# Optimization experiments

Hardware: AMD Instinct MI355X
Metric: run time of the kernel (lower is better)

The kernel has to match this reference:

```python
import jax, jax.numpy as jnp
from jax import lax
import numpy as np

B, T = 256, 64
VOCAB, EMB, UNITS = 10000, 256, 512


def _lstm(x, mask, Wi, Wh, b, reverse, return_sequences):
    # x: [B,T,D], mask: [B,T] bool. Keras LSTM: act=tanh, rec_act=sigmoid,
    # gate order i,f,c,o. Masked steps carry state (output = previous output).
    Bsz = x.shape[0]
    U = Wh.shape[0]
    xw = jnp.einsum('btd,dg->btg', x, Wi) + b  # precompute input projections

    def step(carry, inp):
        h, c = carry
        xw_t, m_t = inp  # [B,4U], [B,1]
        z = xw_t + h @ Wh
        i, f, g, o = jnp.split(z, 4, axis=-1)
        c_new = jax.nn.sigmoid(f) * c + jax.nn.sigmoid(i) * jnp.tanh(g)
        h_new = jax.nn.sigmoid(o) * jnp.tanh(c_new)
        h = jnp.where(m_t, h_new, h)
        c = jnp.where(m_t, c_new, c)
        return (h, c), h

    init = (jnp.zeros((Bsz, U), x.dtype), jnp.zeros((Bsz, U), x.dtype))
    xs = (xw.transpose(1, 0, 2), mask.T[:, :, None])
    (h, _), ys = lax.scan(step, init, xs, reverse=reverse)
    return ys.transpose(1, 0, 2) if return_sequences else h


def _bilstm(x, mask, fwd, bwd, return_sequences):
    yf = _lstm(x, mask, *fwd, reverse=False, return_sequences=return_sequences)
    yb = _lstm(x, mask, *bwd, reverse=True, return_sequences=return_sequences)
    return jnp.concatenate([yf, yb], axis=-1)


def setup_inputs() -> dict:
    key = jax.random.key(0)
    ks = jax.random.split(key, 24)
    g = lambda k, shp, s=0.05: jax.random.normal(k, shp, dtype=jnp.float32) * s
    d = {
        'encoder_output': jax.random.normal(ks[0], (B, 10, 10, 2048), dtype=jnp.float32),
        'sequences': jax.random.randint(ks[1], (B, T), 0, VOCAB),
        'emb': g(ks[2], (VOCAB, EMB)),
        'l1f_Wi': g(ks[3], (EMB, 4 * UNITS)), 'l1f_Wh': g(ks[4], (UNITS, 4 * UNITS)), 'l1f_b': jnp.zeros((4 * UNITS,), jnp.float32),
        'l1b_Wi': g(ks[5], (EMB, 4 * UNITS)), 'l1b_Wh': g(ks[6], (UNITS, 4 * UNITS)), 'l1b_b': jnp.zeros((4 * UNITS,), jnp.float32),
        'l2f_Wi': g(ks[7], (2 * UNITS, 4 * UNITS)), 'l2f_Wh': g(ks[8], (UNITS, 4 * UNITS)), 'l2f_b': jnp.zeros((4 * UNITS,), jnp.float32),
        'l2b_Wi': g(ks[9], (2 * UNITS, 4 * UNITS)), 'l2b_Wh': g(ks[10], (UNITS, 4 * UNITS)), 'l2b_b': jnp.zeros((4 * UNITS,), jnp.float32),
        'W1': g(ks[11], (2048 + 2 * UNITS, 1024)), 'b1': jnp.zeros((1024,), jnp.float32),
        'W2': g(ks[12], (1024, 512)), 'b2': jnp.zeros((512,), jnp.float32),
        'W3': g(ks[13], (512, 1)), 'b3': jnp.zeros((1,), jnp.float32),
    }
    return d


def reference(encoder_output, sequences, emb,
              l1f_Wi, l1f_Wh, l1f_b, l1b_Wi, l1b_Wh, l1b_b,
              l2f_Wi, l2f_Wh, l2f_b, l2b_Wi, l2b_Wh, l2b_b,
              W1, b1, W2, b2, W3, b3):
    # training=False: all dropout layers are identity.
    pooled = jnp.mean(encoder_output, axis=(1, 2))  # [B, 2048]
    mask = sequences != 0                            # mask_zero=True
    tok = emb[sequences]                             # [B,T,EMB]
    lstm1_out = _bilstm(tok, mask, (l1f_Wi, l1f_Wh, l1f_b), (l1b_Wi, l1b_Wh, l1b_b), True)
    lstm2_out = _bilstm(lstm1_out, mask, (l2f_Wi, l2f_Wh, l2f_b), (l2b_Wi, l2b_Wh, l2b_b), False)
    feats = jnp.concatenate([pooled, lstm2_out], axis=1)  # [B, 3072]
    x = jax.nn.relu(feats @ W1 + b1)
    x = jax.nn.relu(x @ W2 + b2)
    return jax.nn.sigmoid(x @ W3 + b3)  # [B,1]
```

## Files before the change

kernel.cpp:

```cpp
#include <hip/hip_runtime.h>
#include <hip/hip_bf16.h>
#include <math.h>

#define BB 256
#define TT 64
#define UU 512
#define XWD 33554432
#define WSTR 520

typedef __hip_bfloat16 bf16;
typedef __attribute__((ext_vector_type(8))) short sh8;
typedef __attribute__((ext_vector_type(4))) short sh4;
typedef __attribute__((ext_vector_type(4))) float floatx4;
typedef __attribute__((ext_vector_type(4))) unsigned int ui4;

__device__ __forceinline__ float bf2f(short s) {
    union { unsigned int u; float f; } v;
    v.u = ((unsigned int)(unsigned short)s) << 16;
    return v.f;
}
__device__ __forceinline__ short f2bf_bits(float f) {
    union { float f; unsigned u; } v; v.f = f;
    unsigned rr = v.u + 0x7fff + ((v.u >> 16) & 1);
    return (short)(rr >> 16);
}
__device__ __forceinline__ float fsig(float x)  { return 1.0f / (1.0f + __expf(-x)); }
__device__ __forceinline__ float ftanh(float x) { return 2.0f / (1.0f + __expf(-2.0f * x)) - 1.0f; }

union U16 { ui4 u; sh8 s; };

__device__ __forceinline__ void coh_load_h8(const bf16* p, sh8 hv[8]) {
    U16 a0, a1, a2, a3, a4, a5, a6, a7;
    asm volatile(
        "global_load_dwordx4 %[o0], %[ad], off sc0 sc1\n\t"
        "global_load_dwordx4 %[o1], %[ad], off offset:64 sc0 sc1\n\t"
        "global_load_dwordx4 %[o2], %[ad], off offset:128 sc0 sc1\n\t"
        "global_load_dwordx4 %[o3], %[ad], off offset:192 sc0 sc1\n\t"
        "global_load_dwordx4 %[o4], %[ad], off offset:256 sc0 sc1\n\t"
        "global_load_dwordx4 %[o5], %[ad], off offset:320 sc0 sc1\n\t"
        "global_load_dwordx4 %[o6], %[ad], off offset:384 sc0 sc1\n\t"
        "global_load_dwordx4 %[o7], %[ad], off offset:448 sc0 sc1\n\t"
        "s_waitcnt vmcnt(0)"
        : [o0]"=&v"(a0.u), [o1]"=&v"(a1.u), [o2]"=&v"(a2.u), [o3]"=&v"(a3.u),
          [o4]"=&v"(a4.u), [o5]"=&v"(a5.u), [o6]"=&v"(a6.u), [o7]"=&v"(a7.u)
        : [ad]"v"(p)
        : "memory");
    hv[0] = a0.s; hv[1] = a1.s; hv[2] = a2.s; hv[3] = a3.s;
    hv[4] = a4.s; hv[5] = a5.s; hv[6] = a6.s; hv[7] = a7.s;
}
__device__ __forceinline__ void coh_store_h(bf16* p, short v) {
    asm volatile("global_store_short %[ad], %[dv], off sc0 sc1"
                 :: [ad]"v"(p), [dv]"v"((unsigned)(unsigned short)v) : "memory");
}
__device__ __forceinline__ void flag_store(unsigned* p, unsigned v) {
    asm volatile("global_store_dword %[ad], %[dv], off sc0 sc1"
                 :: [ad]"v"(p), [dv]"v"(v) : "memory");
}
__device__ __forceinline__ unsigned flag_load(const unsigned* p) {
    unsigned v;
    asm volatile("global_load_dword %[dv], %[ad], off sc0 sc1\n\t"
                 "s_waitcnt vmcnt(0)"
                 : [dv]"=&v"(v) : [ad]"v"(p) : "memory");
    return v;
}

#define GLDS(gp, lp) __builtin_amdgcn_global_load_lds( \
    (const __attribute__((address_space(1))) unsigned int*)(const void*)(gp), \
    (__attribute__((address_space(3))) unsigned int*)(void*)(lp), 16, 0, 0)

__global__ void transpose_conv_kernel(const float* __restrict__ in, bf16* __restrict__ out,
                                      int K, int N, int out_stride) {
    __shared__ float tile[32][33];
    int k0 = blockIdx.y * 32;
    int n0 = blockIdx.x * 32;
    int tid = threadIdx.x;
    int nn = tid & 31, kk = tid >> 5;
    #pragma unroll
    for (int j = 0; j < 4; ++j)
        tile[kk + j * 8][nn] = in[(size_t)(k0 + kk + j * 8) * N + n0 + nn];
    __syncthreads();
    int kk2 = tid & 31, nn2 = tid >> 5;
    #pragma unroll
    for (int j = 0; j < 4; ++j)
        out[(size_t)(n0 + nn2 + j * 8) * out_stride + k0 + kk2] =
            __float2bfloat16(tile[kk2][nn2 + j * 8]);
}

__global__ void pool_kernel(const float* __restrict__ enc, float* __restrict__ pooled) {
    int b = blockIdx.y;
    int e = blockIdx.x * 256 + threadIdx.x;
    const float* p = enc + (size_t)b * 100 * 2048 + e;
    float s = 0.f;
    #pragma unroll 4
    for (int i = 0; i < 100; ++i) s += p[(size_t)i * 2048];
    pooled[(size_t)b * 2048 + e] = s * 0.01f;
}

__global__ void embed_kernel(const int* __restrict__ seq, const float* __restrict__ emb,
                             bf16* __restrict__ tok) {
    int i = blockIdx.x;
    int e = threadIdx.x;
    int b = i >> 6, t = i & 63;
    tok[((size_t)t * BB + b) * 256 + e] = __float2bfloat16(emb[(size_t)seq[i] * 256 + e]);
}

__global__ __launch_bounds__(256)
void gemm_tile(const bf16* __restrict__ A, const bf16* __restrict__ Wt,
               const float* __restrict__ bias, bf16* __restrict__ out,
               int M, int N, int K, int relu, int mode) {
    __shared__ __align__(16) bf16 As[128 * 32];
    __shared__ __align__(16) bf16 Bs[128 * 32];
    const int tid = threadIdx.x;
    const int w = tid >> 6, lane = tid & 63;
    const int lm = lane & 15, q = lane >> 4;
    const int m0 = blockIdx.y * 128;
    const int n0 = blockIdx.x * 128;
    const int wm = (w & 1) * 64, wn = (w >> 1) * 64;

    const int srow = tid >> 2;
    const int sk8  = (tid & 3) * 8;
    const bf16* ga0 = A  + (size_t)(m0 + srow) * K + sk8;
    const bf16* ga1 = A  + (size_t)(m0 + 64 + srow) * K + sk8;
    const bf16* gb0 = Wt + (size_t)(n0 + srow) * K + sk8;
    const bf16* gb1 = Wt + (size_t)(n0 + 64 + srow) * K + sk8;
    bf16* la0 = As + tid * 8;
    bf16* la1 = As + 2048 + tid * 8;
    bf16* lb0 = Bs + tid * 8;
    bf16* lb1 = Bs + 2048 + tid * 8;

    floatx4 acc[4][4];
    #pragma unroll
    for (int i = 0; i < 4; ++i)
        #pragma unroll
        for (int j = 0; j < 4; ++j) acc[i][j] = (floatx4){0.f, 0.f, 0.f, 0.f};

    const bf16* ra[4];
    const bf16* rb[4];
    #pragma unroll
    for (int i = 0; i < 4; ++i) ra[i] = As + (wm + i * 16 + lm) * 32 + q * 8;
    #pragma unroll
    for (int j = 0; j < 4; ++j) rb[j] = Bs + (wn + j * 16 + lm) * 32 + q * 8;

    for (int k0 = 0; k0 < K; k0 += 32) {
        GLDS(ga0 + k0, la0);
        GLDS(ga1 + k0, la1);
        GLDS(gb0 + k0, lb0);
        GLDS(gb1 + k0, lb1);
        __syncthreads();
        sh8 af[4], bfr[4];
        #pragma unroll
        for (int i = 0; i < 4; ++i) af[i] = *(const sh8*)ra[i];
        #pragma unroll
        for (int j = 0; j < 4; ++j) bfr[j] = *(const sh8*)rb[j];
        #pragma unroll
        for (int i = 0; i < 4; ++i)
            #pragma unroll
            for (int j = 0; j < 4; ++j)
                acc[i][j] = __builtin_amdgcn_mfma_f32_16x16x32_bf16(af[i], bfr[j], acc[i][j], 0, 0, 0);
        __syncthreads();
    }

    if (mode == 0) {
        #pragma unroll
        for (int i = 0; i < 4; ++i)
            #pragma unroll
            for (int j = 0; j < 4; ++j) {
                int n = n0 + wn + j * 16 + lm;
                float bv = bias[n];
                #pragma unroll
                for (int r = 0; r < 4; ++r) {
                    int m = m0 + wm + i * 16 + q * 4 + r;
                    float v = acc[i][j][r] + bv;
                    if (relu) v = fmaxf(v, 0.f);
                    out[(size_t)m * N + n] = __float2bfloat16(v);
                }
            }
    } else {
        #pragma unroll
        for (int i = 0; i < 4; ++i) {
            int mb = m0 + wm + i * 16 + q * 4;
            int t = mb >> 8;
            int bq = (mb >> 2) & 63;
            #pragma unroll
            for (int j = 0; j < 4; ++j) {
                int n = n0 + wn + j * 16 + lm;
                float bv = bias[n];
                size_t base = ((((size_t)(t * 64 + bq) * 32 + ((n >> 4) & 31)) * 16
                               + (n & 15)) * 16) + (n >> 9) * 4;
                sh4 sv;
                #pragma unroll
                for (int r = 0; r < 4; ++r)
                    sv[r] = f2bf_bits(acc[i][j][r] + bv);
                *(sh4*)(out + base) = sv;
            }
        }
    }
}

__device__ __forceinline__ void bar_arrive(unsigned* myflag, unsigned val) {
    __syncthreads();
    if (threadIdx.x == 0) flag_store(myflag, val);
}
__device__ __forceinline__ void bar_wait(unsigned* flagbase, unsigned target) {
    if (threadIdx.x < 64) {
        unsigned* my = flagbase + (threadIdx.x & 31);
        for (;;) {
            unsigned v = flag_load(my);
            if (__all(v >= target)) break;
            __builtin_amdgcn_s_sleep(1);
        }
    }
    __syncthreads();
}

__global__ __launch_bounds__(512, 2)
void lstm_seq(const bf16* __restrict__ xw, const bf16* __restrict__ Wht,
              const int* __restrict__ seq, bf16* __restrict__ h0b,
              bf16* __restrict__ h1b, bf16* __restrict__ seqout,
              unsigned* __restrict__ gflags, int tbase) {
    const int dir = blockIdx.z;
    const int u0 = blockIdx.x * 16;
    const int tid = threadIdx.x;
    const int w = tid >> 6, lane = tid & 63;
    const int lm = lane & 15, q = lane >> 4;
    const int kh = w >> 2;
    const int wb = w & 3;
    const int b0blk = blockIdx.y * 64;
    const int b0w = b0blk + wb * 16;
    unsigned* flagbase = gflags + (blockIdx.z * 4 + blockIdx.y) * 32;
    unsigned* myflag   = flagbase + blockIdx.x;

    __shared__ float part[4 * 64 * 17];
    __shared__ __align__(16) bf16 lW[64 * WSTR];
    __shared__ int sq[TT * 64];

    const size_t hdb = (size_t)dir * BB * UU;
    const int koff = kh * 256;
    const bf16* Wd = Wht + (size_t)dir * 2048 * UU;

    for (int i = tid; i < TT * 64; i += 512) {
        int tt = i >> 6, bb = i & 63;
        sq[i] = seq[(b0blk + bb) * TT + tt];
    }
    {
        int row = tid >> 3;
        int ck  = (tid & 7) * 64;
        int g = row >> 4, lmr = row & 15;
        const bf16* gsrc = Wd + (size_t)(g * UU + u0 + lmr) * UU + ck;
        bf16* ldst = lW + row * WSTR + ck;
        #pragma unroll
        for (int j = 0; j < 8; ++j)
            *(sh8*)(ldst + j * 8) = *(const sh8*)(gsrc + j * 8);
    }
    __syncthreads();

    const bf16* lwp0 = lW + (0 * 16 + lm) * WSTR + q * 8 + koff;
    const bf16* lwp1 = lW + (1 * 16 + lm) * WSTR + q * 8 + koff;
    const bf16* lwp2 = lW + (2 * 16 + lm) * WSTR + q * 8 + koff;
    const bf16* lwp3 = lW + (3 * 16 + lm) * WSTR + q * 8 + koff;

    float creg[4] = {0.f, 0.f, 0.f, 0.f};
    float hreg[4] = {0.f, 0.f, 0.f, 0.f};

    sh8 x0p = (sh8)0, x1p = (sh8)0;
    if (kh == 0) {
        const int t0s = dir ? (TT - 1) : 0;
        const bf16* xwp = xw + (size_t)dir * XWD
            + (((size_t)(t0s * 64 + (b0w >> 2) + q) * 32 + (u0 >> 4)) * 16 + lm) * 16;
        x0p = *(const sh8*)xwp;
        x1p = *(const sh8*)(xwp + 8);
    }

    for (int s = 0; s < TT; ++s) {
        const int t = dir ? (TT - 1 - s) : s;
        const bf16* hin = (s & 1) ? h1b : h0b;
        bf16*      hout = (s & 1) ? h0b : h1b;

        if (s) bar_wait(flagbase, (unsigned)(tbase + s));

        const bf16* hA = hin + hdb + (size_t)(b0w + lm) * UU + q * 8 + koff;
        sh8 hv[8];
        coh_load_h8(hA, hv);

        floatx4 acc0, acc1, acc2, acc3;
        if (kh == 0) {
            acc0 = (floatx4){bf2f(x0p[0]), bf2f(x0p[1]), bf2f(x0p[2]), bf2f(x0p[3])};
            acc1 = (floatx4){bf2f(x0p[4]), bf2f(x0p[5]), bf2f(x0p[6]), bf2f(x0p[7])};
            acc2 = (floatx4){bf2f(x1p[0]), bf2f(x1p[1]), bf2f(x1p[2]), bf2f(x1p[3])};
            acc3 = (floatx4){bf2f(x1p[4]), bf2f(x1p[5]), bf2f(x1p[6]), bf2f(x1p[7])};
        } else {
            acc0 = acc1 = acc2 = acc3 = (floatx4){0.f, 0.f, 0.f, 0.f};
        }

        #pragma unroll
        for (int kc = 0; kc < 8; ++kc) {
            sh8 a0 = *(const sh8*)(lwp0 + kc * 32);
            sh8 a1 = *(const sh8*)(lwp1 + kc * 32);
            sh8 a2 = *(const sh8*)(lwp2 + kc * 32);
            sh8 a3 = *(const sh8*)(lwp3 + kc * 32);
            acc0 = __builtin_amdgcn_mfma_f32_16x16x32_bf16(hv[kc], a0, acc0, 0, 0, 0);
            acc1 = __builtin_amdgcn_mfma_f32_16x16x32_bf16(hv[kc], a1, acc1, 0, 0, 0);
            acc2 = __builtin_amdgcn_mfma_f32_16x16x32_bf16(hv[kc], a2, acc2, 0, 0, 0);
            acc3 = __builtin_amdgcn_mfma_f32_16x16x32_bf16(hv[kc], a3, acc3, 0, 0, 0);
        }

        if (kh == 1) {
            float* pp = part + (wb * 64 + lane) * 17;
            #pragma unroll
            for (int r = 0; r < 4; ++r) {
                pp[r] = acc0[r]; pp[4 + r] = acc1[r];
                pp[8 + r] = acc2[r]; pp[12 + r] = acc3[r];
            }
        }
        __syncthreads();
        if (kh == 0) {
            const float* pp = part + (wb * 64 + lane) * 17;
            #pragma unroll
            for (int r = 0; r < 4; ++r) {
                acc0[r] += pp[r]; acc1[r] += pp[4 + r];
                acc2[r] += pp[8 + r]; acc3[r] += pp[12 + r];
            }
            const int uu = u0 + lm;
            #pragma unroll
            for (int r = 0; r < 4; ++r) {
                int b = b0w + q * 4 + r;
                bool m = (sq[t * 64 + wb * 16 + q * 4 + r] != 0);
                float cp = creg[r];
                float cn = fsig(acc1[r]) * cp + fsig(acc0[r]) * ftanh(acc2[r]);
                float hn = fsig(acc3[r]) * ftanh(cn);
                float hv2 = m ? hn : hreg[r];
                creg[r] = m ? cn : cp;
                hreg[r] = hv2;
                size_t off = hdb + (size_t)b * UU + uu;
                short hb = f2bf_bits(hv2);
                coh_store_h(&hout[off], hb);
                if (seqout)
                    __builtin_nontemporal_store(hb,
                        (short*)&seqout[((size_t)t * BB + b) * 1024 + dir * UU + uu]);
            }
        }
        bar_arrive(myflag, (unsigned)(tbase + s + 1));

        if (kh == 0 && s + 1 < TT) {
            const int tn = dir ? (TT - 2 - s) : (s + 1);
            const bf16* xwp = xw + (size_t)dir * XWD
                + (((size_t)(tn * 64 + (b0w >> 2) + q) * 32 + (u0 >> 4)) * 16 + lm) * 16;
            x0p = *(const sh8*)xwp;
            x1p = *(const sh8*)(xwp + 8);
        }
    }
}

__global__ void concat_kernel(const float* __restrict__ pooled, const bf16* __restrict__ h2,
                              bf16* __restrict__ feats) {
    int b = blockIdx.x;
    for (int j = threadIdx.x; j < 3072; j += 256) {
        bf16 v;
        if (j < 2048) v = __float2bfloat16(pooled[(size_t)b * 2048 + j]);
        else {
            int u = j - 2048;
            int dir = u >> 9;
            int uu = u & 511;
            v = h2[((size_t)dir * BB + b) * UU + uu];
        }
        feats[(size_t)b * 3072 + j] = v;
    }
}

__global__ void final_kernel(const bf16* __restrict__ x2, const float* __restrict__ W3,
                             const float* __restrict__ b3, float* __restrict__ out) {
    int b = blockIdx.x;
    int tid = threadIdx.x;
    float v = __bfloat162float(x2[(size_t)b * 512 + tid]) * W3[tid]
            + __bfloat162float(x2[(size_t)b * 512 + 256 + tid]) * W3[256 + tid];
    for (int off = 32; off > 0; off >>= 1) v += __shfl_down(v, off, 64);
    __shared__ float wsum[4];
    if ((tid & 63) == 0) wsum[tid >> 6] = v;
    __syncthreads();
    if (tid == 0) {
        float sum = wsum[0] + wsum[1] + wsum[2] + wsum[3] + b3[0];
        out[b] = 1.0f / (1.0f + expf(-sum));
    }
}

extern "C" void kernel_launch(void* const* d_in, const int* in_sizes, int n_in,
                              void* d_out, int out_size, void* d_ws, size_t ws_size,
                              hipStream_t stream) {
    const float* enc    = (const float*)d_in[0];
    const int*   seq    = (const int*)  d_in[1];
    const float* emb    = (const float*)d_in[2];
    const float* l1f_Wi = (const float*)d_in[3];
    const float* l1f_Wh = (const float*)d_in[4];
    const float* l1f_b  = (const float*)d_in[5];
    const float* l1b_Wi = (const float*)d_in[6];
    const float* l1b_Wh = (const float*)d_in[7];
    const float* l1b_b  = (const float*)d_in[8];
    const float* l2f_Wi = (const float*)d_in[9];
    const float* l2f_Wh = (const float*)d_in[10];
    const float* l2f_b  = (const float*)d_in[11];
    const float* l2b_Wi = (const float*)d_in[12];
    const float* l2b_Wh = (const float*)d_in[13];
    const float* l2b_b  = (const float*)d_in[14];
    const float* W1     = (const float*)d_in[15];
    const float* b1     = (const float*)d_in[16];
    const float* W2     = (const float*)d_in[17];
    const float* b2     = (const float*)d_in[18];
    const float* W3     = (const float*)d_in[19];
    const float* b3     = (const float*)d_in[20];

    char* p = (char*)d_ws;
    bf16* tok      = (bf16*)p;  p += (size_t)TT * BB * 256 * 2;
    bf16* lstm1out = (bf16*)p;  p += (size_t)TT * BB * 1024 * 2;
    bf16* xw       = (bf16*)p;  p += (size_t)2 * XWD * 2;
    bf16* Wh1t     = (bf16*)p;  p += (size_t)2 * 2048 * 512 * 2;
    bf16* Wh2t     = (bf16*)p;  p += (size_t)2 * 2048 * 512 * 2;
    bf16* Wi1t     = (bf16*)p;  p += (size_t)2 * 2048 * 256 * 2;
    bf16* Wi2t     = (bf16*)p;  p += (size_t)2 * 2048 * 1024 * 2;
    bf16* W1t      = (bf16*)p;  p += (size_t)1024 * 3072 * 2;
    bf16* W2t      = (bf16*)p;  p += (size_t)512 * 1024 * 2;
    float* pooled  = (float*)p; p += (size_t)BB * 2048 * 4;
    bf16* feats    = (bf16*)p;  p += (size_t)BB * 3072 * 2;
    bf16* x1       = (bf16*)p;  p += (size_t)BB * 1024 * 2;
    bf16* x2       = (bf16*)p;  p += (size_t)BB * 512 * 2;
    bf16* hb0      = (bf16*)p;  p += (size_t)2 * BB * UU * 2;
    bf16* hb1      = (bf16*)p;  p += (size_t)2 * BB * UU * 2;
    unsigned* gflags = (unsigned*)p; p += 8 * 128;

    hipMemsetAsync(gflags, 0, 8 * 128, stream);

    transpose_conv_kernel<<<dim3(64, 16), 256, 0, stream>>>(l1f_Wh, Wh1t,                    512, 2048, 512);
    transpose_conv_kernel<<<dim3(64, 16), 256, 0, stream>>>(l1b_Wh, Wh1t + (size_t)2048*512, 512, 2048, 512);
    transpose_conv_kernel<<<dim3(64, 16), 256, 0, stream>>>(l2f_Wh, Wh2t,                    512, 2048, 512);
    transpose_conv_kernel<<<dim3(64, 16), 256, 0, stream>>>(l2b_Wh, Wh2t + (size_t)2048*512, 512, 2048, 512);
    transpose_conv_kernel<<<dim3(64, 8),  256, 0, stream>>>(l1f_Wi, Wi1t,                    256, 2048, 256);
    transpose_conv_kernel<<<dim3(64, 8),  256, 0, stream>>>(l1b_Wi, Wi1t + (size_t)2048*256, 256, 2048, 256);
    transpose_conv_kernel<<<dim3(64, 32), 256, 0, stream>>>(l2f_Wi, Wi2t,                     1024, 2048, 1024);
    transpose_conv_kernel<<<dim3(64, 32), 256, 0, stream>>>(l2b_Wi, Wi2t + (size_t)2048*1024, 1024, 2048, 1024);
    transpose_conv_kernel<<<dim3(32, 96), 256, 0, stream>>>(W1, W1t, 3072, 1024, 3072);
    transpose_conv_kernel<<<dim3(16, 32), 256, 0, stream>>>(W2, W2t, 1024, 512, 1024);

    pool_kernel<<<dim3(8, BB), 256, 0, stream>>>(enc, pooled);
    embed_kernel<<<dim3(BB * TT), 256, 0, stream>>>(seq, emb, tok);

    hipMemsetAsync(hb0, 0, (size_t)2 * BB * UU * 2, stream);
    gemm_tile<<<dim3(16, 128), 256, 0, stream>>>(tok, Wi1t,                    l1f_b, xw,       16384, 2048, 256, 0, 2);
    gemm_tile<<<dim3(16, 128), 256, 0, stream>>>(tok, Wi1t + (size_t)2048*256, l1b_b, xw + XWD, 16384, 2048, 256, 0, 2);
    lstm_seq<<<dim3(32, 4, 2), 512, 0, stream>>>(xw, Wh1t, seq, hb0, hb1, lstm1out, gflags, 0);

    hipMemsetAsync(hb0, 0, (size_t)2 * BB * UU * 2, stream);
    gemm_tile<<<dim3(16, 128), 256, 0, stream>>>(lstm1out, Wi2t,                     l2f_b, xw,       16384, 2048, 1024, 0, 2);
    gemm_tile<<<dim3(16, 128), 256, 0, stream>>>(lstm1out, Wi2t + (size_t)2048*1024, l2b_b, xw + XWD, 16384, 2048, 1024, 0, 2);
    lstm_seq<<<dim3(32, 4, 2), 512, 0, stream>>>(xw, Wh2t, seq, hb0, hb1, nullptr, gflags, TT);

    concat_kernel<<<dim3(BB), 256, 0, stream>>>(pooled, hb0, feats);
    gemm_tile<<<dim3(8, 2), 256, 0, stream>>>(feats, W1t, b1, x1, BB, 1024, 3072, 1, 0);
    gemm_tile<<<dim3(4, 2), 256, 0, stream>>>(x1, W2t, b2, x2, BB, 512, 1024, 1, 0);
    final_kernel<<<dim3(BB), 256, 0, stream>>>(x2, W3, b3, (float*)d_out);
}
```

Before: 1.505 ms.

## Per-wave flag polling, deeper xw prefetch, and deferred sequence-output stores

Each wave now polls the global step flags itself instead of wave 0 polling and then a block-wide __syncthreads, which removes one block barrier per timestep. The input-projection prefetch is doubled to two timesteps ahead so the global load latency is better hidden. The nontemporal stores of the sequence output are moved after the flag arrive, which shortens the critical path before other blocks are released. In exchange, all waves hammer the flag memory (more polling traffic) and the kernel holds more registers for the second prefetch buffer.

```diff
diff --git a/kernel.cpp b/kernel.cpp
--- a/kernel.cpp
+++ b/kernel.cpp
@@ -201,16 +201,13 @@
     __syncthreads();
     if (threadIdx.x == 0) flag_store(myflag, val);
 }
-__device__ __forceinline__ void bar_wait(unsigned* flagbase, unsigned target) {
-    if (threadIdx.x < 64) {
-        unsigned* my = flagbase + (threadIdx.x & 31);
-        for (;;) {
-            unsigned v = flag_load(my);
-            if (__all(v >= target)) break;
-            __builtin_amdgcn_s_sleep(1);
-        }
-    }
-    __syncthreads();
+__device__ __forceinline__ void bar_wait_wave(unsigned* flagbase, unsigned target) {
+    unsigned* my = flagbase + (threadIdx.x & 31);
+    for (;;) {
+        unsigned v = flag_load(my);
+        if (__all(v >= target)) break;
+        __builtin_amdgcn_s_sleep(1);
+    }
 }
 
 __global__ __launch_bounds__(512, 2)
@@ -262,13 +259,17 @@
     float creg[4] = {0.f, 0.f, 0.f, 0.f};
     float hreg[4] = {0.f, 0.f, 0.f, 0.f};
 
-    sh8 x0p = (sh8)0, x1p = (sh8)0;
+    sh8 xA0 = (sh8)0, xA1 = (sh8)0, xB0 = (sh8)0, xB1 = (sh8)0;
+    const size_t xwbase = (size_t)dir * XWD;
     if (kh == 0) {
-        const int t0s = dir ? (TT - 1) : 0;
-        const bf16* xwp = xw + (size_t)dir * XWD
-            + (((size_t)(t0s * 64 + (b0w >> 2) + q) * 32 + (u0 >> 4)) * 16 + lm) * 16;
-        x0p = *(const sh8*)xwp;
-        x1p = *(const sh8*)(xwp + 8);
+        const int ta = dir ? (TT - 1) : 0;
+        const int tb = dir ? (TT - 2) : 1;
+        const bf16* pa = xw + xwbase
+            + (((size_t)(ta * 64 + (b0w >> 2) + q) * 32 + (u0 >> 4)) * 16 + lm) * 16;
+        const bf16* pb = xw + xwbase
+            + (((size_t)(tb * 64 + (b0w >> 2) + q) * 32 + (u0 >> 4)) * 16 + lm) * 16;
+        xA0 = *(const sh8*)pa;  xA1 = *(const sh8*)(pa + 8);
+        xB0 = *(const sh8*)pb;  xB1 = *(const sh8*)(pb + 8);
     }
 
     for (int s = 0; s < TT; ++s) {
@@ -276,7 +277,7 @@
         const bf16* hin = (s & 1) ? h1b : h0b;
         bf16*      hout = (s & 1) ? h0b : h1b;
 
-        if (s) bar_wait(flagbase, (unsigned)(tbase + s));
+        if (s) bar_wait_wave(flagbase, (unsigned)(tbase + s));
 
         const bf16* hA = hin + hdb + (size_t)(b0w + lm) * UU + q * 8 + koff;
         sh8 hv[8];
@@ -284,10 +285,10 @@
 
         floatx4 acc0, acc1, acc2, acc3;
         if (kh == 0) {
-            acc0 = (floatx4){bf2f(x0p[0]), bf2f(x0p[1]), bf2f(x0p[2]), bf2f(x0p[3])};
-            acc1 = (floatx4){bf2f(x0p[4]), bf2f(x0p[5]), bf2f(x0p[6]), bf2f(x0p[7])};
-            acc2 = (floatx4){bf2f(x1p[0]), bf2f(x1p[1]), bf2f(x1p[2]), bf2f(x1p[3])};
-            acc3 = (floatx4){bf2f(x1p[4]), bf2f(x1p[5]), bf2f(x1p[6]), bf2f(x1p[7])};
+            acc0 = (floatx4){bf2f(xA0[0]), bf2f(xA0[1]), bf2f(xA0[2]), bf2f(xA0[3])};
+            acc1 = (floatx4){bf2f(xA0[4]), bf2f(xA0[5]), bf2f(xA0[6]), bf2f(xA0[7])};
+            acc2 = (floatx4){bf2f(xA1[0]), bf2f(xA1[1]), bf2f(xA1[2]), bf2f(xA1[3])};
+            acc3 = (floatx4){bf2f(xA1[4]), bf2f(xA1[5]), bf2f(xA1[6]), bf2f(xA1[7])};
         } else {
             acc0 = acc1 = acc2 = acc3 = (floatx4){0.f, 0.f, 0.f, 0.f};
         }
@@ -313,6 +314,7 @@
             }
         }
         __syncthreads();
+        short hbits[4] = {0, 0, 0, 0};
         if (kh == 0) {
             const float* pp = part + (wb * 64 + lane) * 17;
             #pragma unroll
@@ -332,21 +334,30 @@
                 creg[r] = m ? cn : cp;
                 hreg[r] = hv2;
                 size_t off = hdb + (size_t)b * UU + uu;
-                short hb = f2bf_bits(hv2);
-                coh_store_h(&hout[off], hb);
-                if (seqout)
-                    __builtin_nontemporal_store(hb,
+                hbits[r] = f2bf_bits(hv2);
+                coh_store_h(&hout[off], hbits[r]);
+            }
+        }
+        bar_arrive(myflag, (unsigned)(tbase + s + 1));
+
+        if (kh == 0) {
+            if (seqout) {
+                const int uu = u0 + lm;
+                #pragma unroll
+                for (int r = 0; r < 4; ++r) {
+                    int b = b0w + q * 4 + r;
+                    __builtin_nontemporal_store(hbits[r],
                         (short*)&seqout[((size_t)t * BB + b) * 1024 + dir * UU + uu]);
-            }
-        }
-        bar_arrive(myflag, (unsigned)(tbase + s + 1));
-
-        if (kh == 0 && s + 1 < TT) {
-            const int tn = dir ? (TT - 2 - s) : (s + 1);
-            const bf16* xwp = xw + (size_t)dir * XWD
-                + (((size_t)(tn * 64 + (b0w >> 2) + q) * 32 + (u0 >> 4)) * 16 + lm) * 16;
-            x0p = *(const sh8*)xwp;
-            x1p = *(const sh8*)(xwp + 8);
+                }
+            }
+            xA0 = xB0; xA1 = xB1;
+            if (s + 2 < TT) {
+                const int tn = dir ? (TT - 3 - s) : (s + 2);
+                const bf16* pb = xw + xwbase
+                    + (((size_t)(tn * 64 + (b0w >> 2) + q) * 32 + (u0 >> 4)) * 16 + lm) * 16;
+                xB0 = *(const sh8*)pb;
+                xB1 = *(const sh8*)(pb + 8);
+            }
         }
     }
 }
```

Measured after the change: 1.529 ms. No clear change (+1.6%).
